# Kernel optimization log

Measured on AMD Instinct MI355X. Metric: run time of the kernel, lower is better.

Reference implementation:

```python
import jax, jax.numpy as jnp
import jax.lax as lax
import numpy as np
import math

B, T_FRAMES, H, W = 32, 8, 14, 14
C, CA = 768, 384
L = H * W + 1


def setup_inputs() -> dict:
    key = jax.random.key(0)
    ks = jax.random.split(key, 7)
    s = 0.02
    return {
        "x": jax.random.normal(ks[0], (B * T_FRAMES, L, C), dtype=jnp.float32),
        "W1": jax.random.normal(ks[1], (CA, C), dtype=jnp.float32) * s,
        "b1": jnp.zeros((CA,), dtype=jnp.float32),
        "conv_w": jax.random.normal(ks[2], (CA, 1, 3, 3, 3), dtype=jnp.float32) * s,
        "conv_b": jnp.zeros((CA,), dtype=jnp.float32),
        "W2": jax.random.normal(ks[3], (C, CA), dtype=jnp.float32) * s,
        "b2": jnp.zeros((C,), dtype=jnp.float32),
        "T": T_FRAMES,
    }


def reference(x, W1, b1, conv_w, conv_b, W2, b2, T):
    BT, Lx, Cx = x.shape
    Bb = BT // T
    Ca = W1.shape[0]
    Hh = Ww = int(round(math.sqrt(Lx - 1)))
    # fc1 on all tokens except CLS: [BT, L-1, Ca]
    h = jnp.einsum("blc,ac->bla", x[:, 1:, :], W1) + b1
    # -> [B, Ca, T, H, W] for depthwise 3d conv (groups = Ca)
    h = h.reshape(Bb, T, Hh, Ww, Ca).transpose(0, 4, 1, 2, 3)
    h = lax.conv_general_dilated(
        h, conv_w,
        window_strides=(1, 1, 1),
        padding=[(1, 1), (1, 1), (1, 1)],
        dimension_numbers=("NCDHW", "OIDHW", "NCDHW"),
        feature_group_count=Ca,
    ) + conv_b[None, :, None, None, None]
    # back to [BT, L-1, Ca]
    h = h.transpose(0, 2, 3, 4, 1).reshape(BT, Lx - 1, Ca)
    # fc2: [BT, L-1, C]
    h = jnp.einsum("bla,ca->blc", h, W2) + b2
    # residual add onto non-CLS tokens
    return x.at[:, 1:, :].add(h)
```

## Files before the change

kernel.cpp:

```cpp
#include <hip/hip_runtime.h>
#include <stdint.h>

#define BTOT   256
#define LX     197
#define CDIM   768
#define CADIM  384
#define TFR    8
#define LM1    196
#define MTOT   50176

typedef unsigned short u16;
typedef short          bf16x8 __attribute__((ext_vector_type(8)));
typedef unsigned short u16x4  __attribute__((ext_vector_type(4)));
typedef unsigned short u16x8  __attribute__((ext_vector_type(8)));
typedef float          f32x4  __attribute__((ext_vector_type(4)));

typedef const __attribute__((address_space(1))) void gvoid_t;
typedef __attribute__((address_space(3))) void       svoid_t;

static __device__ __forceinline__ u16 f2bf(float f) {
  union { float f; uint32_t u; } v; v.f = f;
  uint32_t u = v.u;
  return (u16)((u + 0x7FFFu + ((u >> 16) & 1u)) >> 16);
}
static __device__ __forceinline__ float bf2f(u16 h) {
  union { uint32_t u; float f; } v; v.u = ((uint32_t)h) << 16;
  return v.f;
}

__global__ void prep_x(const float4* __restrict__ x, u16x4* __restrict__ xb,
                       float4* __restrict__ out, int nvec) {
  int stride = gridDim.x * blockDim.x;
  for (int i = blockIdx.x * blockDim.x + threadIdx.x; i < nvec; i += stride) {
    float4 v = x[i];
    u16x4 o;
    o[0] = f2bf(v.x); o[1] = f2bf(v.y); o[2] = f2bf(v.z); o[3] = f2bf(v.w);
    xb[i] = o;
    int rem = i % 37824;
    if (rem < 192) out[i] = v;
  }
}

__global__ void prep_w(const float* __restrict__ W1, const float* __restrict__ W2,
                       const float* __restrict__ cw, u16* __restrict__ w1b,
                       u16* __restrict__ w2b, float* __restrict__ cwT) {
  int i = blockIdx.x * blockDim.x + threadIdx.x;
  if (i < CADIM * CDIM) { w1b[i] = f2bf(W1[i]); w2b[i] = f2bf(W2[i]); }
  if (i < CADIM * 27) {
    int a = i / 27; int tap = i - a * 27;
    cwT[tap * CADIM + a] = cw[i];
  }
}


__global__ __launch_bounds__(256) void fc1_gemm(
    const u16* __restrict__ A,
    const u16* __restrict__ Bw,
    const float* __restrict__ bias,
    u16* __restrict__ Hout)
{
  __shared__ __align__(16) u16 As[128 * 64];
  __shared__ __align__(16) u16 Bs[128 * 64];
  const int tid  = threadIdx.x;
  const int lane = tid & 63;
  const int wave = tid >> 6;
  const int m0 = blockIdx.x * 128;
  const int n0 = blockIdx.y * 128;
  const int lm = lane & 15;
  const int lk = lane >> 4;
  const int wm = (wave & 1) * 64;
  const int wn = (wave >> 1) * 64;

  const int srow = lane >> 3;
  const int cch  = (lane & 7) ^ srow;
  size_t aoff[4], boff[4];
  u16 *asdst[4], *bsdst[4];
#pragma unroll
  for (int s = 0; s < 4; ++s) {
    int row = wave * 32 + s * 8 + srow;
    int tok = m0 + row;
    int bt = tok / LM1;
    int l = tok - bt * LM1;
    aoff[s] = (size_t)(bt * LX + 1 + l) * CDIM + cch * 8;
    boff[s] = (size_t)(n0 + row) * CDIM + cch * 8;
    asdst[s] = As + (wave * 32 + s * 8) * 64;
    bsdst[s] = Bs + (wave * 32 + s * 8) * 64;
  }
  const int r7  = lm & 7;
  const int sw0 = ((lk    ) ^ r7) << 3;
  const int sw1 = ((lk + 4) ^ r7) << 3;

  f32x4 acc[4][4];
#pragma unroll
  for (int i = 0; i < 4; i++)
#pragma unroll
    for (int j = 0; j < 4; j++) acc[i][j] = (f32x4)0.0f;

  for (int k0 = 0; k0 < CDIM; k0 += 64) {
#pragma unroll
    for (int s = 0; s < 4; ++s) {
      __builtin_amdgcn_global_load_lds((gvoid_t*)(A + aoff[s] + k0),
                                       (svoid_t*)asdst[s], 16, 0, 0);
      __builtin_amdgcn_global_load_lds((gvoid_t*)(Bw + boff[s] + k0),
                                       (svoid_t*)bsdst[s], 16, 0, 0);
    }
    __syncthreads();
    {
      bf16x8 af[4], bfr[4];
#pragma unroll
      for (int i = 0; i < 4; i++)
        af[i] = *(const bf16x8*)&As[(wm + i * 16 + lm) * 64 + sw0];
#pragma unroll
      for (int j = 0; j < 4; j++)
        bfr[j] = *(const bf16x8*)&Bs[(wn + j * 16 + lm) * 64 + sw0];
#pragma unroll
      for (int i = 0; i < 4; i++)
#pragma unroll
        for (int j = 0; j < 4; j++)
          acc[i][j] = __builtin_amdgcn_mfma_f32_16x16x32_bf16(af[i], bfr[j], acc[i][j], 0, 0, 0);
#pragma unroll
      for (int i = 0; i < 4; i++)
        af[i] = *(const bf16x8*)&As[(wm + i * 16 + lm) * 64 + sw1];
#pragma unroll
      for (int j = 0; j < 4; j++)
        bfr[j] = *(const bf16x8*)&Bs[(wn + j * 16 + lm) * 64 + sw1];
#pragma unroll
      for (int i = 0; i < 4; i++)
#pragma unroll
        for (int j = 0; j < 4; j++)
          acc[i][j] = __builtin_amdgcn_mfma_f32_16x16x32_bf16(af[i], bfr[j], acc[i][j], 0, 0, 0);
    }
    __syncthreads();
  }

#pragma unroll
  for (int i = 0; i < 4; i++) {
    int rbase = m0 + wm + i * 16 + lk * 4;
#pragma unroll
    for (int j = 0; j < 4; j++) {
      int col = n0 + wn + j * 16 + lm;
      float bv = bias[col];
#pragma unroll
      for (int r = 0; r < 4; r++)
        Hout[(rbase + r) * CADIM + col] = f2bf(acc[i][j][r] + bv);
    }
  }
}

__global__ __launch_bounds__(256) void dwconv(
    const u16* __restrict__ h1, const float* __restrict__ cwT,
    const float* __restrict__ cb, u16* __restrict__ h2)
{
  int idx = blockIdx.x * blockDim.x + threadIdx.x;
  int cg = idx % 48;
  int rest = idx / 48;
  int wp = rest % 7; rest /= 7;
  int hp = rest % 7; rest /= 7;
  int t = rest & 7;
  int frame = rest;
  int a0 = cg * 8;
  int h0 = hp * 2, w0 = wp * 2;

  float acc[2][2][8];
#pragma unroll
  for (int c = 0; c < 8; ++c) {
    float bv = cb[a0 + c];
    acc[0][0][c] = bv; acc[0][1][c] = bv; acc[1][0][c] = bv; acc[1][1][c] = bv;
  }

#pragma unroll
  for (int dt = -1; dt <= 1; ++dt) {
    int tt = t + dt;
    if (tt < 0 || tt >= TFR) continue;
    float wreg[9][8];
#pragma unroll
    for (int j = 0; j < 9; ++j) {
      const float* wp8 = cwT + ((dt + 1) * 9 + j) * CADIM + a0;
#pragma unroll
      for (int c = 0; c < 8; ++c) wreg[j][c] = wp8[c];
    }
    const u16* fbase = h1 + (size_t)(frame + dt) * LM1 * CADIM + a0;
#pragma unroll
    for (int ih = 0; ih < 4; ++ih) {
      int hh = h0 - 1 + ih;
      if (hh < 0 || hh >= 14) continue;
#pragma unroll
      for (int iw = 0; iw < 4; ++iw) {
        int ww = w0 - 1 + iw;
        if (ww < 0 || ww >= 14) continue;
        bf16x8 v = *(const bf16x8*)(fbase + (hh * 14 + ww) * CADIM);
        float vf[8];
#pragma unroll
        for (int c = 0; c < 8; ++c) vf[c] = bf2f((u16)v[c]);
#pragma unroll
        for (int oh = 0; oh < 2; ++oh) {
          if (ih - 1 - oh < -1 || ih - 1 - oh > 1) continue;
#pragma unroll
          for (int ow = 0; ow < 2; ++ow) {
            if (iw - 1 - ow < -1 || iw - 1 - ow > 1) continue;
            int j = (ih - oh) * 3 + (iw - ow);
#pragma unroll
            for (int c = 0; c < 8; ++c)
              acc[oh][ow][c] += vf[c] * wreg[j][c];
          }
        }
      }
    }
  }
  const size_t obase = (size_t)frame * LM1 * CADIM + a0;
#pragma unroll
  for (int oh = 0; oh < 2; ++oh)
#pragma unroll
    for (int ow = 0; ow < 2; ++ow) {
      u16x8 o;
#pragma unroll
      for (int c = 0; c < 8; ++c) o[c] = f2bf(acc[oh][ow][c]);
      *(u16x8*)(h2 + obase + ((size_t)(h0 + oh) * 14 + w0 + ow) * CADIM) = o;
    }
}

__global__ __launch_bounds__(256) void fc2_gemm(
    const u16* __restrict__ A,
    const u16* __restrict__ Bw,
    const float* __restrict__ bias,
    const float* __restrict__ x,
    float* __restrict__ out)
{
  __shared__ __align__(16) u16 As[128 * 64];
  __shared__ __align__(16) u16 Bs[128 * 64];
  const int tid  = threadIdx.x;
  const int lane = tid & 63;
  const int wave = tid >> 6;
  const int m0 = blockIdx.x * 128;
  const int n0 = blockIdx.y * 128;
  const int lm = lane & 15;
  const int lk = lane >> 4;
  const int wm = (wave & 1) * 64;
  const int wn = (wave >> 1) * 64;

  const int srow = lane >> 3;
  const int cch  = (lane & 7) ^ srow;
  size_t aoff[4], boff[4];
  u16 *asdst[4], *bsdst[4];
#pragma unroll
  for (int s = 0; s < 4; ++s) {
    int row = wave * 32 + s * 8 + srow;
    aoff[s] = (size_t)(m0 + row) * CADIM + cch * 8;
    boff[s] = (size_t)(n0 + row) * CADIM + cch * 8;
    asdst[s] = As + (wave * 32 + s * 8) * 64;
    bsdst[s] = Bs + (wave * 32 + s * 8) * 64;
  }
  const int r7  = lm & 7;
  const int sw0 = ((lk    ) ^ r7) << 3;
  const int sw1 = ((lk + 4) ^ r7) << 3;

  f32x4 acc[4][4];
#pragma unroll
  for (int i = 0; i < 4; i++)
#pragma unroll
    for (int j = 0; j < 4; j++) acc[i][j] = (f32x4)0.0f;

  for (int k0 = 0; k0 < CADIM; k0 += 64) {
#pragma unroll
    for (int s = 0; s < 4; ++s) {
      __builtin_amdgcn_global_load_lds((gvoid_t*)(A + aoff[s] + k0),
                                       (svoid_t*)asdst[s], 16, 0, 0);
      __builtin_amdgcn_global_load_lds((gvoid_t*)(Bw + boff[s] + k0),
                                       (svoid_t*)bsdst[s], 16, 0, 0);
    }
    __syncthreads();
    {
      bf16x8 af[4], bfr[4];
#pragma unroll
      for (int i = 0; i < 4; i++)
        af[i] = *(const bf16x8*)&As[(wm + i * 16 + lm) * 64 + sw0];
#pragma unroll
      for (int j = 0; j < 4; j++)
        bfr[j] = *(const bf16x8*)&Bs[(wn + j * 16 + lm) * 64 + sw0];
#pragma unroll
      for (int i = 0; i < 4; i++)
#pragma unroll
        for (int j = 0; j < 4; j++)
          acc[i][j] = __builtin_amdgcn_mfma_f32_16x16x32_bf16(af[i], bfr[j], acc[i][j], 0, 0, 0);
#pragma unroll
      for (int i = 0; i < 4; i++)
        af[i] = *(const bf16x8*)&As[(wm + i * 16 + lm) * 64 + sw1];
#pragma unroll
      for (int j = 0; j < 4; j++)
        bfr[j] = *(const bf16x8*)&Bs[(wn + j * 16 + lm) * 64 + sw1];
#pragma unroll
      for (int i = 0; i < 4; i++)
#pragma unroll
        for (int j = 0; j < 4; j++)
          acc[i][j] = __builtin_amdgcn_mfma_f32_16x16x32_bf16(af[i], bfr[j], acc[i][j], 0, 0, 0);
    }
    __syncthreads();
  }

#pragma unroll
  for (int i = 0; i < 4; i++) {
    int rbase = m0 + wm + i * 16 + lk * 4;
#pragma unroll
    for (int r = 0; r < 4; r++) {
      int tok = rbase + r;
      int bt = tok / LM1;
      int l = tok - bt * LM1;
      size_t orow = (size_t)(bt * LX + 1 + l) * CDIM;
#pragma unroll
      for (int j = 0; j < 4; j++) {
        int col = n0 + wn + j * 16 + lm;
        out[orow + col] = x[orow + col] + acc[i][j][r] + bias[col];
      }
    }
  }
}

extern "C" void kernel_launch(void* const* d_in, const int* in_sizes, int n_in,
                              void* d_out, int out_size, void* d_ws, size_t ws_size,
                              hipStream_t stream) {
  const float* x  = (const float*)d_in[0];
  const float* W1 = (const float*)d_in[1];
  const float* b1 = (const float*)d_in[2];
  const float* cw = (const float*)d_in[3];
  const float* cb = (const float*)d_in[4];
  const float* W2 = (const float*)d_in[5];
  const float* b2 = (const float*)d_in[6];
  float* out = (float*)d_out;

  char* ws = (char*)d_ws;
  u16*   xb  = (u16*)(ws + 0);
  u16*   w1b = (u16*)(ws + 77463552);
  u16*   w2b = (u16*)(ws + 78053376);
  float* cwT = (float*)(ws + 78643200);
  u16*   h1  = (u16*)(ws + 78684672);
  u16*   h2  = (u16*)(ws + 117219840);

  const int xelems = BTOT * LX * CDIM;

  prep_x  <<<4096, 256, 0, stream>>>((const float4*)x, (u16x4*)xb, (float4*)out, xelems / 4);
  prep_w  <<<(CADIM * CDIM + 255) / 256, 256, 0, stream>>>(W1, W2, cw, w1b, w2b, cwT);
  fc1_gemm<<<dim3(MTOT / 128, CADIM / 128), 256, 0, stream>>>(xb, w1b, b1, h1);
  dwconv  <<<(BTOT * 49 * 48) / 256, 256, 0, stream>>>(h1, cwT, cb, h2);
  fc2_gemm<<<dim3(MTOT / 128, CDIM / 128), 256, 0, stream>>>(h2, w2b, b2, x, out);
}
```

Baseline: 473.2 us.

## Double-buffer LDS in fc1/fc2 GEMMs with BK=32 and batch fc2 epilogue loads

Both GEMMs switch from a single 64-wide K tile to two 32-wide LDS buffers. The next tile's global_load_lds is issued before computing on the current one, so only one barrier per iteration remains and load latency overlaps with MFMA work. The LDS swizzle and addressing are reworked for the 32-wide layout. The fc2 epilogue hoists the bias loads and issues all residual x loads before the stores. The trade-off is less MFMA work per barrier and a more complex indexing scheme that has to stay conflict-free and correct.

```diff
diff --git a/kernel.cpp b/kernel.cpp
--- a/kernel.cpp
+++ b/kernel.cpp
@@ -53,14 +53,41 @@
 }
 
 
+#define GEMM_STAGE(bufidx, k0)                                             \
+  {                                                                        \
+    _Pragma("unroll")                                                      \
+    for (int s = 0; s < 2; ++s) {                                          \
+      __builtin_amdgcn_global_load_lds((gvoid_t*)(A + aoff[s] + (k0)),     \
+          (svoid_t*)(As + (bufidx) * 4096 + ldst[s]), 16, 0, 0);           \
+      __builtin_amdgcn_global_load_lds((gvoid_t*)(Bw + boff[s] + (k0)),    \
+          (svoid_t*)(Bs + (bufidx) * 4096 + ldst[s]), 16, 0, 0);           \
+    }                                                                      \
+  }
+
+#define GEMM_COMPUTE(bufidx)                                               \
+  {                                                                        \
+    const u16* Ab = As + (bufidx) * 4096;                                  \
+    const u16* Bb = Bs + (bufidx) * 4096;                                  \
+    bf16x8 af[4], bfr[4];                                                  \
+    _Pragma("unroll")                                                      \
+    for (int i = 0; i < 4; i++) af[i] = *(const bf16x8*)&Ab[abase + i * 512]; \
+    _Pragma("unroll")                                                      \
+    for (int j = 0; j < 4; j++) bfr[j] = *(const bf16x8*)&Bb[bbase + j * 512]; \
+    _Pragma("unroll")                                                      \
+    for (int i = 0; i < 4; i++)                                            \
+      _Pragma("unroll")                                                    \
+      for (int j = 0; j < 4; j++)                                          \
+        acc[i][j] = __builtin_amdgcn_mfma_f32_16x16x32_bf16(af[i], bfr[j], acc[i][j], 0, 0, 0); \
+  }
+
 __global__ __launch_bounds__(256) void fc1_gemm(
     const u16* __restrict__ A,
     const u16* __restrict__ Bw,
     const float* __restrict__ bias,
     u16* __restrict__ Hout)
 {
-  __shared__ __align__(16) u16 As[128 * 64];
-  __shared__ __align__(16) u16 Bs[128 * 64];
+  __shared__ __align__(16) u16 As[2 * 128 * 32];
+  __shared__ __align__(16) u16 Bs[2 * 128 * 32];
   const int tid  = threadIdx.x;
   const int lane = tid & 63;
   const int wave = tid >> 6;
@@ -71,24 +98,26 @@
   const int wm = (wave & 1) * 64;
   const int wn = (wave >> 1) * 64;
 
-  const int srow = lane >> 3;
-  const int cch  = (lane & 7) ^ srow;
-  size_t aoff[4], boff[4];
-  u16 *asdst[4], *bsdst[4];
-#pragma unroll
-  for (int s = 0; s < 4; ++s) {
-    int row = wave * 32 + s * 8 + srow;
+  const int u   = (lane & 7) ^ (lane >> 3);
+  const int rr  = 2 * (lane >> 3) + (u >> 2);
+  const int cko = (u & 3) * 8;
+  size_t aoff[2], boff[2];
+  int ldst[2];
+#pragma unroll
+  for (int s = 0; s < 2; ++s) {
+    int row = wave * 32 + s * 16 + rr;
     int tok = m0 + row;
     int bt = tok / LM1;
-    int l = tok - bt * LM1;
-    aoff[s] = (size_t)(bt * LX + 1 + l) * CDIM + cch * 8;
-    boff[s] = (size_t)(n0 + row) * CDIM + cch * 8;
-    asdst[s] = As + (wave * 32 + s * 8) * 64;
-    bsdst[s] = Bs + (wave * 32 + s * 8) * 64;
-  }
-  const int r7  = lm & 7;
-  const int sw0 = ((lk    ) ^ r7) << 3;
-  const int sw1 = ((lk + 4) ^ r7) << 3;
+    int l  = tok - bt * LM1;
+    aoff[s] = (size_t)(bt * LX + 1 + l) * CDIM + cko;
+    boff[s] = (size_t)(n0 + row) * CDIM + cko;
+    ldst[s] = (wave * 16 + s * 8) * 64;
+  }
+
+  const int lmh   = lm >> 1;
+  const int slotp = (((lm & 1) << 2) | lk) ^ lmh;
+  const int abase = ((wm >> 1) + lmh) * 64 + slotp * 8;
+  const int bbase = ((wn >> 1) + lmh) * 64 + slotp * 8;
 
   f32x4 acc[4][4];
 #pragma unroll
@@ -96,42 +125,16 @@
 #pragma unroll
     for (int j = 0; j < 4; j++) acc[i][j] = (f32x4)0.0f;
 
-  for (int k0 = 0; k0 < CDIM; k0 += 64) {
-#pragma unroll
-    for (int s = 0; s < 4; ++s) {
-      __builtin_amdgcn_global_load_lds((gvoid_t*)(A + aoff[s] + k0),
-                                       (svoid_t*)asdst[s], 16, 0, 0);
-      __builtin_amdgcn_global_load_lds((gvoid_t*)(Bw + boff[s] + k0),
-                                       (svoid_t*)bsdst[s], 16, 0, 0);
-    }
+  GEMM_STAGE(0, 0);
+  __syncthreads();
+  int cur = 0;
+  for (int kt = 0; kt < 23; ++kt) {
+    GEMM_STAGE(cur ^ 1, (kt + 1) * 32);
+    GEMM_COMPUTE(cur);
     __syncthreads();
-    {
-      bf16x8 af[4], bfr[4];
-#pragma unroll
-      for (int i = 0; i < 4; i++)
-        af[i] = *(const bf16x8*)&As[(wm + i * 16 + lm) * 64 + sw0];
-#pragma unroll
-      for (int j = 0; j < 4; j++)
-        bfr[j] = *(const bf16x8*)&Bs[(wn + j * 16 + lm) * 64 + sw0];
-#pragma unroll
-      for (int i = 0; i < 4; i++)
-#pragma unroll
-        for (int j = 0; j < 4; j++)
-          acc[i][j] = __builtin_amdgcn_mfma_f32_16x16x32_bf16(af[i], bfr[j], acc[i][j], 0, 0, 0);
-#pragma unroll
-      for (int i = 0; i < 4; i++)
-        af[i] = *(const bf16x8*)&As[(wm + i * 16 + lm) * 64 + sw1];
-#pragma unroll
-      for (int j = 0; j < 4; j++)
-        bfr[j] = *(const bf16x8*)&Bs[(wn + j * 16 + lm) * 64 + sw1];
-#pragma unroll
-      for (int i = 0; i < 4; i++)
-#pragma unroll
-        for (int j = 0; j < 4; j++)
-          acc[i][j] = __builtin_amdgcn_mfma_f32_16x16x32_bf16(af[i], bfr[j], acc[i][j], 0, 0, 0);
-    }
-    __syncthreads();
-  }
+    cur ^= 1;
+  }
+  GEMM_COMPUTE(cur);
 
 #pragma unroll
   for (int i = 0; i < 4; i++) {
@@ -226,8 +229,8 @@
     const float* __restrict__ x,
     float* __restrict__ out)
 {
-  __shared__ __align__(16) u16 As[128 * 64];
-  __shared__ __align__(16) u16 Bs[128 * 64];
+  __shared__ __align__(16) u16 As[2 * 128 * 32];
+  __shared__ __align__(16) u16 Bs[2 * 128 * 32];
   const int tid  = threadIdx.x;
   const int lane = tid & 63;
   const int wave = tid >> 6;
@@ -238,21 +241,23 @@
   const int wm = (wave & 1) * 64;
   const int wn = (wave >> 1) * 64;
 
-  const int srow = lane >> 3;
-  const int cch  = (lane & 7) ^ srow;
-  size_t aoff[4], boff[4];
-  u16 *asdst[4], *bsdst[4];
-#pragma unroll
-  for (int s = 0; s < 4; ++s) {
-    int row = wave * 32 + s * 8 + srow;
-    aoff[s] = (size_t)(m0 + row) * CADIM + cch * 8;
-    boff[s] = (size_t)(n0 + row) * CADIM + cch * 8;
-    asdst[s] = As + (wave * 32 + s * 8) * 64;
-    bsdst[s] = Bs + (wave * 32 + s * 8) * 64;
-  }
-  const int r7  = lm & 7;
-  const int sw0 = ((lk    ) ^ r7) << 3;
-  const int sw1 = ((lk + 4) ^ r7) << 3;
+  const int u   = (lane & 7) ^ (lane >> 3);
+  const int rr  = 2 * (lane >> 3) + (u >> 2);
+  const int cko = (u & 3) * 8;
+  size_t aoff[2], boff[2];
+  int ldst[2];
+#pragma unroll
+  for (int s = 0; s < 2; ++s) {
+    int row = wave * 32 + s * 16 + rr;
+    aoff[s] = (size_t)(m0 + row) * CADIM + cko;
+    boff[s] = (size_t)(n0 + row) * CADIM + cko;
+    ldst[s] = (wave * 16 + s * 8) * 64;
+  }
+
+  const int lmh   = lm >> 1;
+  const int slotp = (((lm & 1) << 2) | lk) ^ lmh;
+  const int abase = ((wm >> 1) + lmh) * 64 + slotp * 8;
+  const int bbase = ((wn >> 1) + lmh) * 64 + slotp * 8;
 
   f32x4 acc[4][4];
 #pragma unroll
@@ -260,58 +265,42 @@
 #pragma unroll
     for (int j = 0; j < 4; j++) acc[i][j] = (f32x4)0.0f;
 
-  for (int k0 = 0; k0 < CADIM; k0 += 64) {
-#pragma unroll
-    for (int s = 0; s < 4; ++s) {
-      __builtin_amdgcn_global_load_lds((gvoid_t*)(A + aoff[s] + k0),
-                                       (svoid_t*)asdst[s], 16, 0, 0);
-      __builtin_amdgcn_global_load_lds((gvoid_t*)(Bw + boff[s] + k0),
-                                       (svoid_t*)bsdst[s], 16, 0, 0);
-    }
+  GEMM_STAGE(0, 0);
+  __syncthreads();
+  int cur = 0;
+  for (int kt = 0; kt < 11; ++kt) {
+    GEMM_STAGE(cur ^ 1, (kt + 1) * 32);
+    GEMM_COMPUTE(cur);
     __syncthreads();
-    {
-      bf16x8 af[4], bfr[4];
-#pragma unroll
-      for (int i = 0; i < 4; i++)
-        af[i] = *(const bf16x8*)&As[(wm + i * 16 + lm) * 64 + sw0];
-#pragma unroll
-      for (int j = 0; j < 4; j++)
-        bfr[j] = *(const bf16x8*)&Bs[(wn + j * 16 + lm) * 64 + sw0];
-#pragma unroll
-      for (int i = 0; i < 4; i++)
-#pragma unroll
-        for (int j = 0; j < 4; j++)
-          acc[i][j] = __builtin_amdgcn_mfma_f32_16x16x32_bf16(af[i], bfr[j], acc[i][j], 0, 0, 0);
-#pragma unroll
-      for (int i = 0; i < 4; i++)
-        af[i] = *(const bf16x8*)&As[(wm + i * 16 + lm) * 64 + sw1];
-#pragma unroll
-      for (int j = 0; j < 4; j++)
-        bfr[j] = *(const bf16x8*)&Bs[(wn + j * 16 + lm) * 64 + sw1];
-#pragma unroll
-      for (int i = 0; i < 4; i++)
-#pragma unroll
-        for (int j = 0; j < 4; j++)
-          acc[i][j] = __builtin_amdgcn_mfma_f32_16x16x32_bf16(af[i], bfr[j], acc[i][j], 0, 0, 0);
-    }
-    __syncthreads();
-  }
-
+    cur ^= 1;
+  }
+  GEMM_COMPUTE(cur);
+
+  float bv[4];
+#pragma unroll
+  for (int j = 0; j < 4; j++) bv[j] = bias[n0 + wn + j * 16 + lm];
 #pragma unroll
   for (int i = 0; i < 4; i++) {
     int rbase = m0 + wm + i * 16 + lk * 4;
+    size_t orow[4];
 #pragma unroll
     for (int r = 0; r < 4; r++) {
       int tok = rbase + r;
       int bt = tok / LM1;
-      int l = tok - bt * LM1;
-      size_t orow = (size_t)(bt * LX + 1 + l) * CDIM;
-#pragma unroll
-      for (int j = 0; j < 4; j++) {
-        int col = n0 + wn + j * 16 + lm;
-        out[orow + col] = x[orow + col] + acc[i][j][r] + bias[col];
-      }
-    }
+      int l  = tok - bt * LM1;
+      orow[r] = (size_t)(bt * LX + 1 + l) * CDIM + (n0 + wn + lm);
+    }
+    float xv[4][4];
+#pragma unroll
+    for (int r = 0; r < 4; r++)
+#pragma unroll
+      for (int j = 0; j < 4; j++)
+        xv[r][j] = x[orow[r] + j * 16];
+#pragma unroll
+    for (int r = 0; r < 4; r++)
+#pragma unroll
+      for (int j = 0; j < 4; j++)
+        out[orow[r] + j * 16] = xv[r][j] + acc[i][j][r] + bv[j];
   }
 }
 
```

Result: no change. 470.3 us (-0.6%).
